# Kernel optimization log

Hardware: AMD Instinct MI355X
Metric: run time of the kernel (lower is better)

## Reference

```python
import jax, jax.numpy as jnp
import numpy as np
from jax import lax

N_HEADS = 8
HEAD_DIM = 64
STATE = N_HEADS * HEAD_DIM  # 512
EPS = 1e-6


def setup_inputs() -> dict:
    key = jax.random.key(0)
    ks = jax.random.split(key, 6)
    B, S, D = 4, 4096, 1024
    x = jax.random.normal(ks[0], (B, S, D), jnp.float32)
    w_in = jax.random.normal(ks[1], (4 * STATE, D), jnp.float32) * 0.02
    conv_w = jax.random.normal(ks[2], (STATE, 1, 4), jnp.float32) * 0.5
    state_weight = jax.random.normal(ks[3], (3 * N_HEADS, HEAD_DIM, HEAD_DIM), jnp.float32) * 0.02
    norm_w = jnp.ones((STATE,), jnp.float32)
    w_out = jax.random.normal(ks[5], (D, STATE), jnp.float32) * 0.02
    return {"x": x, "w_in": w_in, "conv_w": conv_w, "state_weight": state_weight, "norm_w": norm_w, "w_out": w_out}


def _forward(x, w_in, conv_w, state_weight, norm_w, w_out):
    B, S, _ = x.shape
    proj = jnp.einsum('bsd,od->bso', x, w_in)  # [B,S,4*STATE]
    xi, xf, xr, g = jnp.split(proj, [STATE, 2 * STATE, 3 * STATE], axis=-1)

    # causal depthwise conv1d on xi (pad left k-1, groups = STATE), then silu
    K = conv_w.shape[-1]
    xi_c = xi.transpose(0, 2, 1)  # [B,C,S]
    xi_c = lax.conv_general_dilated(xi_c, conv_w, window_strides=(1,),
                                    padding=[(K - 1, 0)], feature_group_count=STATE)
    xi = jax.nn.silu(xi_c.transpose(0, 2, 1))  # [B,S,STATE]

    xi = xi.reshape(B, S, N_HEADS, HEAD_DIM)
    xf = xf.reshape(B, S, N_HEADS, HEAD_DIM)
    xr = xr.reshape(B, S, N_HEADS, HEAD_DIM)

    W = state_weight[:N_HEADS]
    Wf = state_weight[N_HEADS:2 * N_HEADS]
    Wr = state_weight[2 * N_HEADS:]

    def step(h, inp):
        xt, xft, xrt = inp  # each [B,N,H]
        f = jax.nn.sigmoid(jnp.einsum('bnh,nhk->bnk', h, Wf) + xft)
        r = jax.nn.sigmoid(jnp.einsum('bnh,nhk->bnk', h, Wr) + xrt)
        z = jnp.tanh(jnp.einsum('bnh,nhk->bnk', h * r, W) + xt)
        h_new = f * h + (1.0 - f) * z
        return h_new, h_new

    h0 = jnp.zeros((B, N_HEADS, HEAD_DIM), x.dtype)
    xs = (xi.transpose(1, 0, 2, 3), xf.transpose(1, 0, 2, 3), xr.transpose(1, 0, 2, 3))
    _, ys = lax.scan(step, h0, xs)  # [S,B,N,H]

    y = ys.transpose(1, 0, 2, 3).reshape(B, S, STATE)
    y = y * jax.nn.silu(g)
    # RMSNorm
    y = y * lax.rsqrt(jnp.mean(y * y, axis=-1, keepdims=True) + EPS) * norm_w
    return jnp.einsum('bss_,os_->bso'.replace('s_', 'c'), y, w_out)


def reference(x, w_in, conv_w, state_weight, norm_w, w_out):
    return _forward(x, w_in, conv_w, state_weight, norm_w, w_out)
```

## Files before the change

### kernel.cpp

```cpp
#include <hip/hip_runtime.h>
#include <hip/hip_bf16.h>
#include <cstddef>

#define B_      4
#define S_      4096
#define D_      1024
#define NH_     8
#define HD_     64
#define STATE_  512
#define PROJ_   2048
#define ROWS_   16384

typedef float f32x4 __attribute__((ext_vector_type(4)));
typedef __bf16 bf16x8 __attribute__((ext_vector_type(8)));
typedef _Float16 f16x2 __attribute__((ext_vector_type(2)));

__device__ __forceinline__ unsigned short bfbits(float f) {
    __hip_bfloat16 h = __float2bfloat16(f);
    return __builtin_bit_cast(unsigned short, h);
}

__device__ __forceinline__ float b2f(unsigned short u) {
    union { unsigned int i; float f; } v;
    v.i = ((unsigned int)u) << 16;
    return v.f;
}

__device__ __forceinline__ float fast_sigmoid(float x) {
    return __builtin_amdgcn_rcpf(1.0f + __expf(-x));
}

__device__ __forceinline__ float fast_tanh(float x) {
    return 1.0f - 2.0f * __builtin_amdgcn_rcpf(__expf(2.0f * x) + 1.0f);
}

__device__ __forceinline__ void async_copy16(void* lds, const void* g) {
    __builtin_amdgcn_global_load_lds(
        (const __attribute__((address_space(1))) unsigned int*)g,
        (__attribute__((address_space(3))) unsigned int*)lds,
        16, 0, 0);
}

__device__ __forceinline__ unsigned int pkf16(float a, float b) {
    auto h = __builtin_amdgcn_cvt_pkrtz(a, b);
    return __builtin_bit_cast(unsigned int, h);
}

__device__ __forceinline__ f16x2 u2h(unsigned int u) {
    return __builtin_bit_cast(f16x2, u);
}

__device__ __forceinline__ f16x2 rl_h2(unsigned int v, int lane) {
    int r = __builtin_amdgcn_readlane((int)v, lane);
    return __builtin_bit_cast(f16x2, r);
}

__device__ __forceinline__ float fdot2f(f16x2 a, f16x2 b, float c) {
    return __builtin_amdgcn_fdot2(a, b, c, false);
}

__device__ __forceinline__ unsigned int pack_pair(float v, bool oddlane) {
    int vb = __builtin_bit_cast(int, v);
    int pb = __builtin_amdgcn_mov_dpp(vb, 0xB1, 0xF, 0xF, true);
    float p = __builtin_bit_cast(float, pb);
    float lo = oddlane ? p : v;
    float hi = oddlane ? v : p;
    return pkf16(lo, hi);
}

__global__ __launch_bounds__(256) void f2bf(const float* __restrict__ in,
                                            unsigned short* __restrict__ out, int n4) {
    int i = blockIdx.x * 256 + threadIdx.x;
    if (i < n4) {
        float4 v = ((const float4*)in)[i];
        ushort4 o;
        o.x = bfbits(v.x); o.y = bfbits(v.y); o.z = bfbits(v.z); o.w = bfbits(v.w);
        ((ushort4*)out)[i] = o;
    }
}

__device__ __forceinline__ void store_out(float* p, float v) { *p = v; }
__device__ __forceinline__ void store_out(__hip_bfloat16* p, float v) { *p = __float2bfloat16(v); }

template <typename OutT>
__global__ __launch_bounds__(256, 1) void gemm_bt(const unsigned short* __restrict__ A,
                                                  const unsigned short* __restrict__ Bm,
                                                  OutT* __restrict__ C,
                                                  int M, int N, int K) {
    __shared__ __align__(16) unsigned short As[128 * 32];
    __shared__ __align__(16) unsigned short Bs[128 * 32];
    const int tid  = threadIdx.x;
    const int lane = tid & 63;
    const int w    = tid >> 6;
    const int wm   = w >> 1;
    const int wn   = w & 1;
    const int l16  = lane & 15;
    const int quad = lane >> 4;
    const int m0 = blockIdx.y * 128;
    const int n0 = blockIdx.x * 128;

    f32x4 acc[4][4] = {};

    const int off0 = w * 1024 + lane * 16;
    const int off1 = (w + 4) * 1024 + lane * 16;
    const int r0 = off0 >> 6, cb0 = off0 & 63;
    const int r1 = off1 >> 6, cb1 = off1 & 63;
    char* lA0 = (char*)As + w * 1024;
    char* lA1 = (char*)As + (w + 4) * 1024;
    char* lB0 = (char*)Bs + w * 1024;
    char* lB1 = (char*)Bs + (w + 4) * 1024;
    const size_t Kb = (size_t)K * 2;

    for (int k0 = 0; k0 < K; k0 += 32) {
        const char* a0 = (const char*)A + (size_t)(m0 + r0) * Kb + (size_t)k0 * 2 + cb0;
        const char* a1 = (const char*)A + (size_t)(m0 + r1) * Kb + (size_t)k0 * 2 + cb1;
        const char* b0 = (const char*)Bm + (size_t)(n0 + r0) * Kb + (size_t)k0 * 2 + cb0;
        const char* b1 = (const char*)Bm + (size_t)(n0 + r1) * Kb + (size_t)k0 * 2 + cb1;
        async_copy16(lA0, a0);
        async_copy16(lA1, a1);
        async_copy16(lB0, b0);
        async_copy16(lB1, b1);
        __syncthreads();

        bf16x8 af[4], bf[4];
#pragma unroll
        for (int mt = 0; mt < 4; ++mt) {
            int r = wm * 64 + mt * 16 + l16;
            af[mt] = *(const bf16x8*)(&As[r * 32 + quad * 8]);
        }
#pragma unroll
        for (int nt = 0; nt < 4; ++nt) {
            int r = wn * 64 + nt * 16 + l16;
            bf[nt] = *(const bf16x8*)(&Bs[r * 32 + quad * 8]);
        }
#pragma unroll
        for (int mt = 0; mt < 4; ++mt)
#pragma unroll
            for (int nt = 0; nt < 4; ++nt)
                acc[mt][nt] = __builtin_amdgcn_mfma_f32_16x16x32_bf16(af[mt], bf[nt], acc[mt][nt], 0, 0, 0);
        __syncthreads();
    }

#pragma unroll
    for (int mt = 0; mt < 4; ++mt) {
#pragma unroll
        for (int nt = 0; nt < 4; ++nt) {
            const int col = n0 + wn * 64 + nt * 16 + l16;
            const int row = m0 + wm * 64 + mt * 16 + quad * 4;
#pragma unroll
            for (int rg = 0; rg < 4; ++rg)
                store_out(&C[(size_t)(row + rg) * N + col], acc[mt][nt][rg]);
        }
    }
}

__global__ __launch_bounds__(256) void transpose_scan(const unsigned short* __restrict__ proj,
                                                      ushort4* __restrict__ sc) {
    const int idx = blockIdx.x * 256 + threadIdx.x;
    const int c   = idx & 511;
    const int row = idx >> 9;
    const int b = row >> 12, t = row & 4095;
    const int n = c >> 6, kk = c & 63;
    const unsigned short* src = proj + (size_t)row * PROJ_ + c;
    ushort4 v;
    v.x = src[0];
    v.y = src[512];
    v.z = src[1024];
    v.w = src[1536];
    sc[((size_t)(b * 8 + n) * S_ + t) * 64 + kk] = v;
}

#define SCAN_STEP(T, V)                                                        \
    {                                                                          \
        const float xi_raw = b2f(V.x);                                         \
        const float xf_v   = b2f(V.y);                                         \
        const float xr_v   = b2f(V.z);                                         \
        const float g_v    = b2f(V.w);                                         \
        {                       \
            const int tn = ((T) + 2 < S_) ? (T) + 2 : S_ - 1;                  \
            V = pin[(size_t)tn * 64];                                          \
        }                                                                      \
        float xc = fmaf(cw3, xi_raw, fmaf(cw2, xm1, fmaf(cw1, xm2, cw0 * xm3)));\
        xm3 = xm2; xm2 = xm1; xm1 = xi_raw;                                    \
        const float xi_v = xc * fast_sigmoid(xc);                              \
        float fa0 = xf_v, fa1 = 0.f, fa2 = 0.f, fa3 = 0.f;                     \
        float ra0 = xr_v, ra1 = 0.f, ra2 = 0.f, ra3 = 0.f;                     \
        _Pragma("unroll")                                                      \
        for (int jp = 0; jp < 32; jp += 4) {                                   \
            const f16x2 h0 = rl_h2(hpk, 2 * jp);                               \
            const f16x2 h1 = rl_h2(hpk, 2 * jp + 2);                           \
            const f16x2 h2 = rl_h2(hpk, 2 * jp + 4);                           \
            const f16x2 h3 = rl_h2(hpk, 2 * jp + 6);                           \
            fa0 = fdot2f(h0, u2h(Wf2[jp]),     fa0);                           \
            ra0 = fdot2f(h0, u2h(Wr2[jp]),     ra0);                           \
            fa1 = fdot2f(h1, u2h(Wf2[jp + 1]), fa1);                           \
            ra1 = fdot2f(h1, u2h(Wr2[jp + 1]), ra1);                           \
            fa2 = fdot2f(h2, u2h(Wf2[jp + 2]), fa2);                           \
            ra2 = fdot2f(h2, u2h(Wr2[jp + 2]), ra2);                           \
            fa3 = fdot2f(h3, u2h(Wf2[jp + 3]), fa3);                           \
            ra3 = fdot2f(h3, u2h(Wr2[jp + 3]), ra3);                           \
        }                                                                      \
        const float f_v = fast_sigmoid((fa0 + fa1) + (fa2 + fa3));             \
        const float r_v = fast_sigmoid((ra0 + ra1) + (ra2 + ra3));             \
        const unsigned int hrpk = pack_pair(h_me * r_v, oddlane);              \
        float za0 = xi_v, za1 = 0.f, za2 = 0.f, za3 = 0.f;                     \
        _Pragma("unroll")                                                      \
        for (int jp = 0; jp < 32; jp += 4) {                                   \
            za0 = fdot2f(rl_h2(hrpk, 2 * jp),     u2h(Wz2[jp]),     za0);      \
            za1 = fdot2f(rl_h2(hrpk, 2 * jp + 2), u2h(Wz2[jp + 1]), za1);      \
            za2 = fdot2f(rl_h2(hrpk, 2 * jp + 4), u2h(Wz2[jp + 2]), za2);      \
            za3 = fdot2f(rl_h2(hrpk, 2 * jp + 6), u2h(Wz2[jp + 3]), za3);      \
        }                                                                      \
        const float z_v = fast_tanh((za0 + za1) + (za2 + za3));                \
        const float hn  = fmaf(f_v, h_me - z_v, z_v);                          \
        h_me = hn;                                                             \
        hpk  = pack_pair(hn, oddlane);                                         \
        yout[(size_t)(T) * STATE_] = hn * (g_v * fast_sigmoid(g_v));           \
    }

__global__ __launch_bounds__(64)
__attribute__((amdgpu_waves_per_eu(1, 1)))
void scan_kernel(
    const ushort4* __restrict__ scanin,
    const float* __restrict__ conv_w,
    const float* __restrict__ sw,
    float* __restrict__ y)
{
    const int bn = blockIdx.x;
    const int b  = bn >> 3;
    const int n  = bn & 7;
    const int k  = threadIdx.x;
    const int c  = n * HD_ + k;
    const bool oddlane = (k & 1) != 0;

    unsigned int Wz2[32], Wf2[32], Wr2[32];
    {
        const float* wz = sw + (size_t)n * 4096 + k;
        const float* wf = wz + 8 * 4096;
        const float* wr = wz + 16 * 4096;
#pragma unroll
        for (int jp = 0; jp < 32; ++jp) {
            Wz2[jp] = pkf16(wz[(2 * jp) * 64], wz[(2 * jp + 1) * 64]);
            Wf2[jp] = pkf16(wf[(2 * jp) * 64], wf[(2 * jp + 1) * 64]);
            Wr2[jp] = pkf16(wr[(2 * jp) * 64], wr[(2 * jp + 1) * 64]);
        }
    }
    const float cw0 = conv_w[c * 4 + 0];
    const float cw1 = conv_w[c * 4 + 1];
    const float cw2 = conv_w[c * 4 + 2];
    const float cw3 = conv_w[c * 4 + 3];

    float h_me = 0.0f;
    unsigned int hpk = 0;
    float xm1 = 0.f, xm2 = 0.f, xm3 = 0.f;

    const ushort4* pin = scanin + (size_t)bn * S_ * 64 + k;
    float* yout = y + (size_t)b * S_ * STATE_ + c;

    ushort4 aV = pin[0];
    ushort4 bV = pin[64];

    for (int t = 0; t < S_; t += 2) {
        SCAN_STEP(t,     aV);
        SCAN_STEP(t + 1, bV);
    }
}

__global__ __launch_bounds__(128) void rmsnorm_bf16(const float* __restrict__ y,
                                                    const float* __restrict__ nw,
                                                    unsigned short* __restrict__ out) {
    const int row = blockIdx.x;
    const int t   = threadIdx.x;
    const float4 v = ((const float4*)(y + (size_t)row * STATE_))[t];
    float ss = fmaf(v.x, v.x, fmaf(v.y, v.y, fmaf(v.z, v.z, v.w * v.w)));
#pragma unroll
    for (int off = 32; off > 0; off >>= 1) ss += __shfl_xor(ss, off, 64);
    __shared__ float wred[2];
    if ((t & 63) == 0) wred[t >> 6] = ss;
    __syncthreads();
    const float tot   = wred[0] + wred[1];
    const float scale = rsqrtf(tot * (1.0f / (float)STATE_) + 1e-6f);
    const float4 w4 = ((const float4*)nw)[t];
    ushort4 o;
    o.x = bfbits(v.x * scale * w4.x);
    o.y = bfbits(v.y * scale * w4.y);
    o.z = bfbits(v.z * scale * w4.z);
    o.w = bfbits(v.w * scale * w4.w);
    ((ushort4*)out)[(size_t)row * (STATE_ / 4) + t] = o;
}

extern "C" void kernel_launch(void* const* d_in, const int* in_sizes, int n_in,
                              void* d_out, int out_size, void* d_ws, size_t ws_size,
                              hipStream_t stream) {
    const float* x      = (const float*)d_in[0];
    const float* w_in   = (const float*)d_in[1];
    const float* conv_w = (const float*)d_in[2];
    const float* sw     = (const float*)d_in[3];
    const float* norm_w = (const float*)d_in[4];
    const float* w_out  = (const float*)d_in[5];
    float* out = (float*)d_out;

    char* ws = (char*)d_ws;
    unsigned short* xbf     = (unsigned short*)(ws + 0);
    unsigned short* w_inbf  = (unsigned short*)(ws + 33554432);
    unsigned short* w_outbf = (unsigned short*)(ws + 37748736);
    ushort4*        scanin  = (ushort4*)(ws + 38797312);
    float*          yf      = (float*)(ws + 0);
    unsigned short* ybf     = (unsigned short*)(ws + 38797312);
    unsigned short* projbf  = (unsigned short*)d_out;

    f2bf<<<(ROWS_ * D_ / 4 + 255) / 256, 256, 0, stream>>>(x, xbf, ROWS_ * D_ / 4);
    f2bf<<<(PROJ_ * D_ / 4 + 255) / 256, 256, 0, stream>>>(w_in, w_inbf, PROJ_ * D_ / 4);
    f2bf<<<(D_ * STATE_ / 4 + 255) / 256, 256, 0, stream>>>(w_out, w_outbf, D_ * STATE_ / 4);

    gemm_bt<__hip_bfloat16><<<dim3(PROJ_ / 128, ROWS_ / 128), 256, 0, stream>>>(
        xbf, w_inbf, (__hip_bfloat16*)projbf, ROWS_, PROJ_, D_);

    transpose_scan<<<ROWS_ * 512 / 256, 256, 0, stream>>>(projbf, scanin);

    scan_kernel<<<32, 64, 0, stream>>>(scanin, conv_w, sw, yf);

    rmsnorm_bf16<<<ROWS_, 128, 0, stream>>>(yf, norm_w, ybf);

    gemm_bt<float><<<dim3(D_ / 128, ROWS_ / 128), 256, 0, stream>>>(
        ybf, w_outbf, out, ROWS_, D_, STATE_);
}
```

Measured before the change: 2.425 ms.

## Split recurrent scan step across two wavefronts with LDS handoff

The scan kernel now runs two waves per (batch, head) block instead of one. Wave 0 computes the forget gate and the state update. Wave 1 computes the reset gate and the candidate matvec, and hands the candidate sum to wave 0 through LDS. The new state comes back through LDS as fp16 pairs. The goal is to take the forget-gate matvec off the serial critical path and halve per-wave weight register pressure, at the cost of two workgroup barriers and LDS round trips on every timestep.

Result: faster. 2.142 ms (-11.7%).

```diff
diff --git a/kernel.cpp b/kernel.cpp
--- a/kernel.cpp
+++ b/kernel.cpp
@@ -66,6 +66,10 @@
     float lo = oddlane ? p : v;
     float hi = oddlane ? v : p;
     return pkf16(lo, hi);
+}
+
+__device__ __forceinline__ void fence_bar() {
+    asm volatile("s_waitcnt lgkmcnt(0)\n\ts_barrier" ::: "memory");
 }
 
 __global__ __launch_bounds__(256) void f2bf(const float* __restrict__ in,
@@ -170,11 +174,17 @@
     sc[((size_t)(b * 8 + n) * S_ + t) * 64 + kk] = v;
 }
 
-#define SCAN_STEP(T, V)                                                        \
+
+#define RD4(Q, P)                                                              \
+    ra0 = fdot2f(u2h(Q.x), u2h(WA2[(P)]),     ra0);                            \
+    ra1 = fdot2f(u2h(Q.y), u2h(WA2[(P) + 1]), ra1);                            \
+    ra2 = fdot2f(u2h(Q.z), u2h(WA2[(P) + 2]), ra2);                            \
+    ra3 = fdot2f(u2h(Q.w), u2h(WA2[(P) + 3]), ra3);
+
+#define W0_STEP(T, V)                                                          \
     {                                                                          \
         const float xi_raw = b2f(V.x);                                         \
         const float xf_v   = b2f(V.y);                                         \
-        const float xr_v   = b2f(V.z);                                         \
         const float g_v    = b2f(V.w);                                         \
         {                       \
             const int tn = ((T) + 2 < S_) ? (T) + 2 : S_ - 1;                  \
@@ -184,41 +194,65 @@
         xm3 = xm2; xm2 = xm1; xm1 = xi_raw;                                    \
         const float xi_v = xc * fast_sigmoid(xc);                              \
         float fa0 = xf_v, fa1 = 0.f, fa2 = 0.f, fa3 = 0.f;                     \
-        float ra0 = xr_v, ra1 = 0.f, ra2 = 0.f, ra3 = 0.f;                     \
         _Pragma("unroll")                                                      \
         for (int jp = 0; jp < 32; jp += 4) {                                   \
             const f16x2 h0 = rl_h2(hpk, 2 * jp);                               \
             const f16x2 h1 = rl_h2(hpk, 2 * jp + 2);                           \
             const f16x2 h2 = rl_h2(hpk, 2 * jp + 4);                           \
             const f16x2 h3 = rl_h2(hpk, 2 * jp + 6);                           \
-            fa0 = fdot2f(h0, u2h(Wf2[jp]),     fa0);                           \
-            ra0 = fdot2f(h0, u2h(Wr2[jp]),     ra0);                           \
-            fa1 = fdot2f(h1, u2h(Wf2[jp + 1]), fa1);                           \
-            ra1 = fdot2f(h1, u2h(Wr2[jp + 1]), ra1);                           \
-            fa2 = fdot2f(h2, u2h(Wf2[jp + 2]), fa2);                           \
-            ra2 = fdot2f(h2, u2h(Wr2[jp + 2]), ra2);                           \
-            fa3 = fdot2f(h3, u2h(Wf2[jp + 3]), fa3);                           \
-            ra3 = fdot2f(h3, u2h(Wr2[jp + 3]), ra3);                           \
+            fa0 = fdot2f(h0, u2h(WA2[jp]),     fa0);                           \
+            fa1 = fdot2f(h1, u2h(WA2[jp + 1]), fa1);                           \
+            fa2 = fdot2f(h2, u2h(WA2[jp + 2]), fa2);                           \
+            fa3 = fdot2f(h3, u2h(WA2[jp + 3]), fa3);                           \
         }                                                                      \
         const float f_v = fast_sigmoid((fa0 + fa1) + (fa2 + fa3));             \
+        fence_bar();                                                 \
+        const float zsum = lds_S[k];                                           \
+        const float z_v  = fast_tanh(zsum + xi_v);                             \
+        const float hn   = fmaf(f_v, h_me - z_v, z_v);                         \
+        h_me = hn;                                                             \
+        hpk  = pack_pair(hn, oddlane);                                         \
+        lds_h[k] = hn;                                                         \
+        if (!oddlane) lds_pairs[k >> 1] = hpk;                                 \
+        yout[(size_t)(T) * STATE_] = hn * (g_v * fast_sigmoid(g_v));           \
+        fence_bar();                                                 \
+    }
+
+#define W1_STEP(T, V)                                                          \
+    {                                                                          \
+        const float xr_v = b2f(V.z);                                           \
+        {                                                                      \
+            const int tn = ((T) + 2 < S_) ? (T) + 2 : S_ - 1;                  \
+            V = pin[(size_t)tn * 64];                                          \
+        }                                                                      \
+        const float h_my = lds_h[k];                                           \
+        const uint4 q0 = *(const uint4*)&lds_pairs[0];                         \
+        const uint4 q1 = *(const uint4*)&lds_pairs[4];                         \
+        const uint4 q2 = *(const uint4*)&lds_pairs[8];                         \
+        const uint4 q3 = *(const uint4*)&lds_pairs[12];                        \
+        const uint4 q4 = *(const uint4*)&lds_pairs[16];                        \
+        const uint4 q5 = *(const uint4*)&lds_pairs[20];                        \
+        const uint4 q6 = *(const uint4*)&lds_pairs[24];                        \
+        const uint4 q7 = *(const uint4*)&lds_pairs[28];                        \
+        float ra0 = xr_v, ra1 = 0.f, ra2 = 0.f, ra3 = 0.f;                     \
+        RD4(q0, 0)  RD4(q1, 4)  RD4(q2, 8)  RD4(q3, 12)                        \
+        RD4(q4, 16) RD4(q5, 20) RD4(q6, 24) RD4(q7, 28)                        \
         const float r_v = fast_sigmoid((ra0 + ra1) + (ra2 + ra3));             \
-        const unsigned int hrpk = pack_pair(h_me * r_v, oddlane);              \
-        float za0 = xi_v, za1 = 0.f, za2 = 0.f, za3 = 0.f;                     \
+        const unsigned int hrpk = pack_pair(h_my * r_v, oddlane);              \
+        float za0 = 0.f, za1 = 0.f, za2 = 0.f, za3 = 0.f;                      \
         _Pragma("unroll")                                                      \
         for (int jp = 0; jp < 32; jp += 4) {                                   \
-            za0 = fdot2f(rl_h2(hrpk, 2 * jp),     u2h(Wz2[jp]),     za0);      \
-            za1 = fdot2f(rl_h2(hrpk, 2 * jp + 2), u2h(Wz2[jp + 1]), za1);      \
-            za2 = fdot2f(rl_h2(hrpk, 2 * jp + 4), u2h(Wz2[jp + 2]), za2);      \
-            za3 = fdot2f(rl_h2(hrpk, 2 * jp + 6), u2h(Wz2[jp + 3]), za3);      \
+            za0 = fdot2f(rl_h2(hrpk, 2 * jp),     u2h(WB2[jp]),     za0);      \
+            za1 = fdot2f(rl_h2(hrpk, 2 * jp + 2), u2h(WB2[jp + 1]), za1);      \
+            za2 = fdot2f(rl_h2(hrpk, 2 * jp + 4), u2h(WB2[jp + 2]), za2);      \
+            za3 = fdot2f(rl_h2(hrpk, 2 * jp + 6), u2h(WB2[jp + 3]), za3);      \
         }                                                                      \
-        const float z_v = fast_tanh((za0 + za1) + (za2 + za3));                \
-        const float hn  = fmaf(f_v, h_me - z_v, z_v);                          \
-        h_me = hn;                                                             \
-        hpk  = pack_pair(hn, oddlane);                                         \
-        yout[(size_t)(T) * STATE_] = hn * (g_v * fast_sigmoid(g_v));           \
-    }
-
-__global__ __launch_bounds__(64)
+        lds_S[k] = (za0 + za1) + (za2 + za3);                                  \
+        fence_bar();                                                 \
+        fence_bar();                                                 \
+    }
+
+__global__ __launch_bounds__(128)
 __attribute__((amdgpu_waves_per_eu(1, 1)))
 void scan_kernel(
     const ushort4* __restrict__ scanin,
@@ -226,23 +260,29 @@
     const float* __restrict__ sw,
     float* __restrict__ y)
 {
+    __shared__ __align__(16) unsigned int lds_pairs[32];
+    __shared__ float lds_h[64];
+    __shared__ float lds_S[64];
+
     const int bn = blockIdx.x;
     const int b  = bn >> 3;
     const int n  = bn & 7;
-    const int k  = threadIdx.x;
+    const int w  = threadIdx.x >> 6;
+    const int k  = threadIdx.x & 63;
     const int c  = n * HD_ + k;
     const bool oddlane = (k & 1) != 0;
 
-    unsigned int Wz2[32], Wf2[32], Wr2[32];
+    unsigned int WA2[32], WB2[32];
     {
-        const float* wz = sw + (size_t)n * 4096 + k;
-        const float* wf = wz + 8 * 4096;
-        const float* wr = wz + 16 * 4096;
-#pragma unroll
-        for (int jp = 0; jp < 32; ++jp) {
-            Wz2[jp] = pkf16(wz[(2 * jp) * 64], wz[(2 * jp + 1) * 64]);
-            Wf2[jp] = pkf16(wf[(2 * jp) * 64], wf[(2 * jp + 1) * 64]);
-            Wr2[jp] = pkf16(wr[(2 * jp) * 64], wr[(2 * jp + 1) * 64]);
+        const float* wa = sw + (size_t)n * 4096 + k + (w == 0 ? 8 * 4096 : 16 * 4096);
+#pragma unroll
+        for (int jp = 0; jp < 32; ++jp)
+            WA2[jp] = pkf16(wa[(2 * jp) * 64], wa[(2 * jp + 1) * 64]);
+        if (w != 0) {
+            const float* wb = sw + (size_t)n * 4096 + k;
+#pragma unroll
+            for (int jp = 0; jp < 32; ++jp)
+                WB2[jp] = pkf16(wb[(2 * jp) * 64], wb[(2 * jp + 1) * 64]);
         }
     }
     const float cw0 = conv_w[c * 4 + 0];
@@ -250,19 +290,30 @@
     const float cw2 = conv_w[c * 4 + 2];
     const float cw3 = conv_w[c * 4 + 3];
 
-    float h_me = 0.0f;
-    unsigned int hpk = 0;
-    float xm1 = 0.f, xm2 = 0.f, xm3 = 0.f;
-
     const ushort4* pin = scanin + (size_t)bn * S_ * 64 + k;
     float* yout = y + (size_t)b * S_ * STATE_ + c;
 
+    if (w == 0) {
+        if (k < 32) lds_pairs[k] = 0u;
+        lds_h[k] = 0.f;
+    }
+    fence_bar();
+
     ushort4 aV = pin[0];
     ushort4 bV = pin[64];
 
-    for (int t = 0; t < S_; t += 2) {
-        SCAN_STEP(t,     aV);
-        SCAN_STEP(t + 1, bV);
+    if (w == 0) {
+        float h_me = 0.0f, xm1 = 0.f, xm2 = 0.f, xm3 = 0.f;
+        unsigned int hpk = 0;
+        for (int t = 0; t < S_; t += 2) {
+            W0_STEP(t,     aV);
+            W0_STEP(t + 1, bV);
+        }
+    } else {
+        for (int t = 0; t < S_; t += 2) {
+            W1_STEP(t,     aV);
+            W1_STEP(t + 1, bV);
+        }
     }
 }
 
@@ -318,7 +369,7 @@
 
     transpose_scan<<<ROWS_ * 512 / 256, 256, 0, stream>>>(projbf, scanin);
 
-    scan_kernel<<<32, 64, 0, stream>>>(scanin, conv_w, sw, yf);
+    scan_kernel<<<32, 128, 0, stream>>>(scanin, conv_w, sw, yf);
 
     rmsnorm_bf16<<<ROWS_, 128, 0, stream>>>(yf, norm_w, ybf);
 
```
